# Kernel tuning notes

Measured on AMD Instinct MI355X. Metric: run time of the kernel, lower is better.

## Reference

```python
import jax, jax.numpy as jnp
import numpy as np

K = 16                 # neighbors
CH = (64, 64, 64)      # edge-MLP channels
C_IN = 64              # input feature channels
EPS = 1e-3             # Keras BatchNormalization default epsilon


def setup_inputs() -> dict:
    key = jax.random.key(0)
    ks = jax.random.split(key, 24)
    B, N = 256, 128
    inp = {}
    inp["points"] = jax.random.normal(ks[0], (B, N, 2), jnp.float32)
    inp["features"] = jax.random.normal(ks[1], (B, N, C_IN), jnp.float32)
    ins = [2 * C_IN, CH[0], CH[1]]
    i = 2
    for l, (cin, cout) in enumerate(zip(ins, CH)):
        inp[f"w{l}"] = jax.random.normal(ks[i], (cin, cout), jnp.float32) / np.sqrt(cin).astype(np.float32); i += 1
        inp[f"g{l}"] = jnp.ones((cout,), jnp.float32)
        inp[f"b{l}"] = jnp.zeros((cout,), jnp.float32)
        inp[f"m{l}"] = 0.1 * jax.random.normal(ks[i], (cout,), jnp.float32); i += 1
        inp[f"v{l}"] = jnp.ones((cout,), jnp.float32)
    inp["wsc"] = jax.random.normal(ks[i], (C_IN, CH[-1]), jnp.float32) / np.sqrt(C_IN).astype(np.float32); i += 1
    inp["gsc"] = jnp.ones((CH[-1],), jnp.float32)
    inp["bsc"] = jnp.zeros((CH[-1],), jnp.float32)
    inp["msc"] = 0.1 * jax.random.normal(ks[i], (CH[-1],), jnp.float32)
    inp["vsc"] = jnp.ones((CH[-1],), jnp.float32)
    return inp


def _bn(x, g, b, m, v):
    # inference-mode BatchNorm over last (channel) axis
    return (x - m) * jax.lax.rsqrt(v + EPS) * g + b


def _forward(points, features, params):
    # pairwise squared distances  [B, N, N]
    r = jnp.sum(points * points, axis=-1, keepdims=True)
    d = r - 2.0 * jnp.einsum('bnd,bmd->bnm', points, points) + jnp.swapaxes(r, 1, 2)
    # k+1 nearest (incl. self), drop self  -> [B, N, K]
    _, idx = jax.lax.top_k(-d, K + 1)
    idx = idx[:, :, 1:]
    # gather neighbor features  [B, N, K, C]
    knn = jax.vmap(lambda f, i: f[i])(features, idx)
    center = features[:, :, None, :]
    # edge features: concat(center, neighbor - center)  [B, N, K, 2C]
    x = jnp.concatenate([jnp.broadcast_to(center, knn.shape), knn - center], axis=-1)
    # edge MLP: 1x1 convs == per-edge matmuls
    for (w, g, b, m, v) in params[:-1]:
        x = jax.nn.relu(_bn(jnp.einsum('bnkc,cd->bnkd', x, w), g, b, m, v))
    pooled = jnp.mean(x, axis=2)                      # [B, N, C_out]
    wsc, gsc, bsc, msc, vsc = params[-1]
    sc = _bn(features @ wsc, gsc, bsc, msc, vsc)      # shortcut 1x1 conv + BN
    return jax.nn.relu(sc + pooled)


def reference(points, features,
              w0, g0, b0, m0, v0,
              w1, g1, b1, m1, v1,
              w2, g2, b2, m2, v2,
              wsc, gsc, bsc, msc, vsc):
    params = [(w0, g0, b0, m0, v0), (w1, g1, b1, m1, v1),
              (w2, g2, b2, m2, v2), (wsc, gsc, bsc, msc, vsc)]
    return _forward(points, features, params)
```

## Files before the change

### kernel.cpp

```cpp
#include <hip/hip_runtime.h>
#include <stdint.h>


#define KK 16
#define EPSV 1e-3f
#define SW0 136
#define SW 72

typedef __bf16 bf16x8 __attribute__((ext_vector_type(8)));
typedef float f32x4 __attribute__((ext_vector_type(4)));
union B8 { uint4 u; bf16x8 v; };

__device__ __forceinline__ unsigned int f2ord(float f) {
  unsigned int u = __float_as_uint(f);
  return (u & 0x80000000u) ? ~u : (u | 0x80000000u);
}
__device__ __forceinline__ unsigned int f2b(float f) {
  unsigned int u = __float_as_uint(f);
  return (u + 0x7FFFu + ((u >> 16) & 1u)) >> 16;
}
__device__ __forceinline__ unsigned int pk(float lo, float hi) {
  return f2b(lo) | (f2b(hi) << 16);
}

__global__ __launch_bounds__(256) void knn_kernel(const float* __restrict__ pts,
                                                  int* __restrict__ knn) {
  __shared__ __align__(16) unsigned long long keys[4][128];
  const int wv = threadIdx.x >> 6;
  const int lane = threadIdx.x & 63;
  const int row = blockIdx.x * 4 + wv;
  const int b = row >> 7;
  const int n = row & 127;
  const float* pb = pts + b * 128 * 2;
  const float xn = pb[2 * n], yn = pb[2 * n + 1];
  const float rn = __fadd_rn(__fmul_rn(xn, xn), __fmul_rn(yn, yn));

  unsigned long long key0, key1;
#pragma unroll
  for (int h = 0; h < 2; ++h) {
    const int j = lane + h * 64;
    const float xj = pb[2 * j], yj = pb[2 * j + 1];
    const float rj = __fadd_rn(__fmul_rn(xj, xj), __fmul_rn(yj, yj));
    const float dot = __fadd_rn(__fmul_rn(xn, xj), __fmul_rn(yn, yj));
    const float d = __fadd_rn(__fsub_rn(rn, __fmul_rn(2.0f, dot)), rj);
    unsigned long long k = ((unsigned long long)f2ord(d) << 32) | (unsigned int)j;
    if (h == 0) key0 = k; else key1 = k;
  }
  keys[wv][lane] = key0;
  keys[wv][lane + 64] = key1;
  int c0 = 0, c1 = 0;
#pragma unroll 8
  for (int j = 0; j < 128; j += 2) {
    const ulonglong2 kp = *(const ulonglong2*)&keys[wv][j];
    c0 += (kp.x < key0); c0 += (kp.y < key0);
    c1 += (kp.x < key1); c1 += (kp.y < key1);
  }
  if (c0 >= 1 && c0 <= 16) knn[row * KK + c0 - 1] = lane;
  if (c1 >= 1 && c1 <= 16) knn[row * KK + c1 - 1] = lane + 64;
}

__global__ __launch_bounds__(256, 2) void mlp_kernel(
    const float* __restrict__ feat, const int* __restrict__ knnIdx,
    const float* __restrict__ w0, const float* __restrict__ g0,
    const float* __restrict__ b0, const float* __restrict__ m0,
    const float* __restrict__ v0, const float* __restrict__ w1,
    const float* __restrict__ g1, const float* __restrict__ b1,
    const float* __restrict__ m1, const float* __restrict__ v1,
    const float* __restrict__ w2, const float* __restrict__ g2,
    const float* __restrict__ b2, const float* __restrict__ m2,
    const float* __restrict__ v2, const float* __restrict__ wsc,
    const float* __restrict__ gsc, const float* __restrict__ bsc,
    const float* __restrict__ msc, const float* __restrict__ vsc,
    float* __restrict__ out) {
  __shared__ __align__(16) unsigned short w0T[64 * SW0];
  __shared__ __align__(16) unsigned short w1T[64 * SW];
  __shared__ __align__(16) unsigned short w2T[64 * SW];
  __shared__ __align__(16) unsigned short wscT[64 * SW];
  __shared__ __align__(16) unsigned short X0[4][16 * SW0];
  __shared__ __align__(16) unsigned short CFB[4][16 * SW];

  const int tid = threadIdx.x;
  const int wv = tid >> 6;
  const int lane = tid & 63;
  const int m = lane & 15;
  const int q4 = lane >> 4;

#pragma unroll
  for (int q = 0; q < 8; ++q) {
    const int v = tid + 256 * q;
    const float4 w = ((const float4*)w0)[v];
    const int i = v >> 4, c = (v & 15) << 2;
    w0T[(c + 0) * SW0 + i] = (unsigned short)f2b(w.x);
    w0T[(c + 1) * SW0 + i] = (unsigned short)f2b(w.y);
    w0T[(c + 2) * SW0 + i] = (unsigned short)f2b(w.z);
    w0T[(c + 3) * SW0 + i] = (unsigned short)f2b(w.w);
  }
#pragma unroll
  for (int q = 0; q < 4; ++q) {
    const int v = tid + 256 * q;
    const int i = v >> 4, c = (v & 15) << 2;
    float4 w = ((const float4*)w1)[v];
    w1T[(c + 0) * SW + i] = (unsigned short)f2b(w.x);
    w1T[(c + 1) * SW + i] = (unsigned short)f2b(w.y);
    w1T[(c + 2) * SW + i] = (unsigned short)f2b(w.z);
    w1T[(c + 3) * SW + i] = (unsigned short)f2b(w.w);
    w = ((const float4*)w2)[v];
    w2T[(c + 0) * SW + i] = (unsigned short)f2b(w.x);
    w2T[(c + 1) * SW + i] = (unsigned short)f2b(w.y);
    w2T[(c + 2) * SW + i] = (unsigned short)f2b(w.z);
    w2T[(c + 3) * SW + i] = (unsigned short)f2b(w.w);
    w = ((const float4*)wsc)[v];
    wscT[(c + 0) * SW + i] = (unsigned short)f2b(w.x);
    wscT[(c + 1) * SW + i] = (unsigned short)f2b(w.y);
    wscT[(c + 2) * SW + i] = (unsigned short)f2b(w.z);
    wscT[(c + 3) * SW + i] = (unsigned short)f2b(w.w);
  }

  float s0[4], o0[4], s1[4], o1[4], s2[4], o2[4], ssc[4], osc[4];
#pragma unroll
  for (int nt = 0; nt < 4; ++nt) {
    const int c = nt * 16 + m;
    float s;
    s = g0[c] / sqrtf(v0[c] + EPSV); s0[nt] = s; o0[nt] = b0[c] - m0[c] * s;
    s = g1[c] / sqrtf(v1[c] + EPSV); s1[nt] = s; o1[nt] = b1[c] - m1[c] * s;
    s = g2[c] / sqrtf(v2[c] + EPSV); s2[nt] = s; o2[nt] = b2[c] - m2[c] * s;
    s = gsc[c] / sqrtf(vsc[c] + EPSV); ssc[nt] = s; osc[nt] = bsc[c] - msc[c] * s;
  }

  const int row0 = blockIdx.x * 64 + wv * 16;
  {
    const int r = lane >> 2, p = lane & 3;
    const float4* fr = (const float4*)(feat + (row0 + r) * 64);
    const float4 a = fr[p * 4 + 0], bq = fr[p * 4 + 1];
    const float4 cq = fr[p * 4 + 2], dq = fr[p * 4 + 3];
    uint4 u0, u1;
    u0.x = pk(a.x, a.y); u0.y = pk(a.z, a.w);
    u0.z = pk(bq.x, bq.y); u0.w = pk(bq.z, bq.w);
    u1.x = pk(cq.x, cq.y); u1.y = pk(cq.z, cq.w);
    u1.z = pk(dq.x, dq.y); u1.w = pk(dq.z, dq.w);
    *(uint4*)&CFB[wv][r * SW + p * 16] = u0;
    *(uint4*)&CFB[wv][r * SW + p * 16 + 8] = u1;
  }
  __syncthreads();

  const f32x4 fzero = {0.f, 0.f, 0.f, 0.f};
  f32x4 sacc[4] = {fzero, fzero, fzero, fzero};
#pragma unroll
  for (int t = 0; t < 2; ++t) {
    B8 af; af.u = *(const uint4*)&CFB[wv][m * SW + t * 32 + q4 * 8];
#pragma unroll
    for (int nt = 0; nt < 4; ++nt) {
      B8 bf_; bf_.u = *(const uint4*)&wscT[(nt * 16 + m) * SW + t * 32 + q4 * 8];
      sacc[nt] = __builtin_amdgcn_mfma_f32_16x16x32_bf16(af.v, bf_.v, sacc[nt], 0, 0, 0);
    }
  }
  float scf[4][4];
#pragma unroll
  for (int nt = 0; nt < 4; ++nt)
#pragma unroll
    for (int r = 0; r < 4; ++r)
      scf[nt][r] = fmaf(sacc[nt][r], ssc[nt], osc[nt]);

  const float* featb = feat + (row0 >> 7) * (128 * 64);
  const int kk = lane >> 2, pp = lane & 3;

  for (int qo = 0; qo < 4; ++qo) {
#pragma unroll
    for (int ri = 0; ri < 4; ++ri) {
      const int rr = qo * 4 + ri;
      const int row = row0 + rr;

      {
        const int j = knnIdx[row * KK + kk];
        const float4* np_ = (const float4*)(featb + j * 64);
        const float4* cp_ = (const float4*)(feat + row * 64);
        const float4 n0 = np_[pp * 4 + 0], n1 = np_[pp * 4 + 1];
        const float4 n2 = np_[pp * 4 + 2], n3 = np_[pp * 4 + 3];
        const float4 c0 = cp_[pp * 4 + 0], c1 = cp_[pp * 4 + 1];
        const float4 c2 = cp_[pp * 4 + 2], c3 = cp_[pp * 4 + 3];
        uint4 u;
        u.x = pk(c0.x, c0.y); u.y = pk(c0.z, c0.w);
        u.z = pk(c1.x, c1.y); u.w = pk(c1.z, c1.w);
        *(uint4*)&X0[wv][kk * SW0 + pp * 16] = u;
        u.x = pk(c2.x, c2.y); u.y = pk(c2.z, c2.w);
        u.z = pk(c3.x, c3.y); u.w = pk(c3.z, c3.w);
        *(uint4*)&X0[wv][kk * SW0 + pp * 16 + 8] = u;
        u.x = pk(n0.x - c0.x, n0.y - c0.y); u.y = pk(n0.z - c0.z, n0.w - c0.w);
        u.z = pk(n1.x - c1.x, n1.y - c1.y); u.w = pk(n1.z - c1.z, n1.w - c1.w);
        *(uint4*)&X0[wv][kk * SW0 + 64 + pp * 16] = u;
        u.x = pk(n2.x - c2.x, n2.y - c2.y); u.y = pk(n2.z - c2.z, n2.w - c2.w);
        u.z = pk(n3.x - c3.x, n3.y - c3.y); u.w = pk(n3.z - c3.z, n3.w - c3.w);
        *(uint4*)&X0[wv][kk * SW0 + 64 + pp * 16 + 8] = u;
      }

      f32x4 acc[4] = {fzero, fzero, fzero, fzero};
#pragma unroll
      for (int t = 0; t < 4; ++t) {
        B8 af; af.u = *(const uint4*)&X0[wv][m * SW0 + t * 32 + q4 * 8];
#pragma unroll
        for (int nt = 0; nt < 4; ++nt) {
          B8 bf_; bf_.u = *(const uint4*)&w0T[(nt * 16 + m) * SW0 + t * 32 + q4 * 8];
          acc[nt] = __builtin_amdgcn_mfma_f32_16x16x32_bf16(af.v, bf_.v, acc[nt], 0, 0, 0);
        }
      }
#pragma unroll
      for (int nt = 0; nt < 4; ++nt)
#pragma unroll
        for (int r2 = 0; r2 < 4; ++r2) {
          const float y = fmaxf(fmaf(acc[nt][r2], s0[nt], o0[nt]), 0.f);
          X0[wv][(q4 * 4 + r2) * SW0 + nt * 16 + m] = (unsigned short)f2b(y);
        }

      acc[0] = fzero; acc[1] = fzero; acc[2] = fzero; acc[3] = fzero;
#pragma unroll
      for (int t = 0; t < 2; ++t) {
        B8 af; af.u = *(const uint4*)&X0[wv][m * SW0 + t * 32 + q4 * 8];
#pragma unroll
        for (int nt = 0; nt < 4; ++nt) {
          B8 bf_; bf_.u = *(const uint4*)&w1T[(nt * 16 + m) * SW + t * 32 + q4 * 8];
          acc[nt] = __builtin_amdgcn_mfma_f32_16x16x32_bf16(af.v, bf_.v, acc[nt], 0, 0, 0);
        }
      }
#pragma unroll
      for (int nt = 0; nt < 4; ++nt)
#pragma unroll
        for (int r2 = 0; r2 < 4; ++r2) {
          const float y = fmaxf(fmaf(acc[nt][r2], s1[nt], o1[nt]), 0.f);
          X0[wv][(q4 * 4 + r2) * SW0 + nt * 16 + m] = (unsigned short)f2b(y);
        }

      acc[0] = fzero; acc[1] = fzero; acc[2] = fzero; acc[3] = fzero;
#pragma unroll
      for (int t = 0; t < 2; ++t) {
        B8 af; af.u = *(const uint4*)&X0[wv][m * SW0 + t * 32 + q4 * 8];
#pragma unroll
        for (int nt = 0; nt < 4; ++nt) {
          B8 bf_; bf_.u = *(const uint4*)&w2T[(nt * 16 + m) * SW + t * 32 + q4 * 8];
          acc[nt] = __builtin_amdgcn_mfma_f32_16x16x32_bf16(af.v, bf_.v, acc[nt], 0, 0, 0);
        }
      }

      float pool[4];
#pragma unroll
      for (int nt = 0; nt < 4; ++nt) {
        float p_ = 0.f;
#pragma unroll
        for (int r2 = 0; r2 < 4; ++r2)
          p_ += fmaxf(fmaf(acc[nt][r2], s2[nt], o2[nt]), 0.f);
        p_ += __shfl_xor(p_, 16);
        p_ += __shfl_xor(p_, 32);
        pool[nt] = p_ * 0.0625f;
      }
      if (q4 == qo) {
#pragma unroll
        for (int nt = 0; nt < 4; ++nt)
          out[row * 64 + nt * 16 + m] = fmaxf(scf[nt][ri] + pool[nt], 0.f);
      }
    }
  }
}

extern "C" void kernel_launch(void* const* d_in, const int* in_sizes, int n_in,
                              void* d_out, int out_size, void* d_ws, size_t ws_size,
                              hipStream_t stream) {
  const float* pts = (const float*)d_in[0];
  const float* feat = (const float*)d_in[1];
  const float* w0 = (const float*)d_in[2];
  const float* g0 = (const float*)d_in[3];
  const float* b0 = (const float*)d_in[4];
  const float* m0 = (const float*)d_in[5];
  const float* v0 = (const float*)d_in[6];
  const float* w1 = (const float*)d_in[7];
  const float* g1 = (const float*)d_in[8];
  const float* b1 = (const float*)d_in[9];
  const float* m1 = (const float*)d_in[10];
  const float* v1 = (const float*)d_in[11];
  const float* w2 = (const float*)d_in[12];
  const float* g2 = (const float*)d_in[13];
  const float* b2 = (const float*)d_in[14];
  const float* m2 = (const float*)d_in[15];
  const float* v2 = (const float*)d_in[16];
  const float* wsc = (const float*)d_in[17];
  const float* gsc = (const float*)d_in[18];
  const float* bsc = (const float*)d_in[19];
  const float* msc = (const float*)d_in[20];
  const float* vsc = (const float*)d_in[21];
  float* out = (float*)d_out;

  int* knn = (int*)d_ws;

  knn_kernel<<<dim3(256 * 128 / 4), dim3(256), 0, stream>>>(pts, knn);
  mlp_kernel<<<dim3(512), dim3(256), 0, stream>>>(
      feat, knn, w0, g0, b0, m0, v0, w1, g1, b1, m1, v1, w2, g2, b2, m2, v2,
      wsc, gsc, bsc, msc, vsc, out);
}
```

Measured before the change: 180.9 us.

## Precompute center term of first edge layer once per point and prefetch neighbor rows

The first edge-MLP layer is split algebraically: concat(c, n-c)·W0 = c·(W0top - W0bot) + n·W0bot. The center contribution is computed once per point with MFMA and broadcast by shuffle, so the per-row layer-0 GEMM drops from K=128 to K=64 and the center feature reload per row goes away. kNN indices are loaded up front and the next neighbor row is software-prefetched while the current one is computed. The bf16 conversion now uses the native cast, and the LDS staging buffer shrinks. The neighbor term is rounded to bf16 directly instead of the difference, which slightly changes numerics, and more registers stay live.

```diff
diff --git a/kernel.cpp b/kernel.cpp
--- a/kernel.cpp
+++ b/kernel.cpp
@@ -15,12 +15,12 @@
   unsigned int u = __float_as_uint(f);
   return (u & 0x80000000u) ? ~u : (u | 0x80000000u);
 }
-__device__ __forceinline__ unsigned int f2b(float f) {
-  unsigned int u = __float_as_uint(f);
-  return (u + 0x7FFFu + ((u >> 16) & 1u)) >> 16;
+__device__ __forceinline__ unsigned short f2bs(float f) {
+  __bf16 b = (__bf16)f;
+  return __builtin_bit_cast(unsigned short, b);
 }
 __device__ __forceinline__ unsigned int pk(float lo, float hi) {
-  return f2b(lo) | (f2b(hi) << 16);
+  return (unsigned int)f2bs(lo) | ((unsigned int)f2bs(hi) << 16);
 }
 
 __global__ __launch_bounds__(256) void knn_kernel(const float* __restrict__ pts,
@@ -31,17 +31,17 @@
   const int row = blockIdx.x * 4 + wv;
   const int b = row >> 7;
   const int n = row & 127;
-  const float* pb = pts + b * 128 * 2;
-  const float xn = pb[2 * n], yn = pb[2 * n + 1];
-  const float rn = __fadd_rn(__fmul_rn(xn, xn), __fmul_rn(yn, yn));
+  const float2* pb = (const float2*)(pts + b * 128 * 2);
+  const float2 pn = pb[n];
+  const float rn = __fadd_rn(__fmul_rn(pn.x, pn.x), __fmul_rn(pn.y, pn.y));
 
   unsigned long long key0, key1;
 #pragma unroll
   for (int h = 0; h < 2; ++h) {
     const int j = lane + h * 64;
-    const float xj = pb[2 * j], yj = pb[2 * j + 1];
-    const float rj = __fadd_rn(__fmul_rn(xj, xj), __fmul_rn(yj, yj));
-    const float dot = __fadd_rn(__fmul_rn(xn, xj), __fmul_rn(yn, yj));
+    const float2 pj = pb[j];
+    const float rj = __fadd_rn(__fmul_rn(pj.x, pj.x), __fmul_rn(pj.y, pj.y));
+    const float dot = __fadd_rn(__fmul_rn(pn.x, pj.x), __fmul_rn(pn.y, pj.y));
     const float d = __fadd_rn(__fsub_rn(rn, __fmul_rn(2.0f, dot)), rj);
     unsigned long long k = ((unsigned long long)f2ord(d) << 32) | (unsigned int)j;
     if (h == 0) key0 = k; else key1 = k;
@@ -76,8 +76,7 @@
   __shared__ __align__(16) unsigned short w1T[64 * SW];
   __shared__ __align__(16) unsigned short w2T[64 * SW];
   __shared__ __align__(16) unsigned short wscT[64 * SW];
-  __shared__ __align__(16) unsigned short X0[4][16 * SW0];
-  __shared__ __align__(16) unsigned short CFB[4][16 * SW];
+  __shared__ __align__(16) unsigned short X0[4][16 * SW];
 
   const int tid = threadIdx.x;
   const int wv = tid >> 6;
@@ -90,30 +89,30 @@
     const int v = tid + 256 * q;
     const float4 w = ((const float4*)w0)[v];
     const int i = v >> 4, c = (v & 15) << 2;
-    w0T[(c + 0) * SW0 + i] = (unsigned short)f2b(w.x);
-    w0T[(c + 1) * SW0 + i] = (unsigned short)f2b(w.y);
-    w0T[(c + 2) * SW0 + i] = (unsigned short)f2b(w.z);
-    w0T[(c + 3) * SW0 + i] = (unsigned short)f2b(w.w);
+    w0T[(c + 0) * SW0 + i] = f2bs(w.x);
+    w0T[(c + 1) * SW0 + i] = f2bs(w.y);
+    w0T[(c + 2) * SW0 + i] = f2bs(w.z);
+    w0T[(c + 3) * SW0 + i] = f2bs(w.w);
   }
 #pragma unroll
   for (int q = 0; q < 4; ++q) {
     const int v = tid + 256 * q;
     const int i = v >> 4, c = (v & 15) << 2;
     float4 w = ((const float4*)w1)[v];
-    w1T[(c + 0) * SW + i] = (unsigned short)f2b(w.x);
-    w1T[(c + 1) * SW + i] = (unsigned short)f2b(w.y);
-    w1T[(c + 2) * SW + i] = (unsigned short)f2b(w.z);
-    w1T[(c + 3) * SW + i] = (unsigned short)f2b(w.w);
+    w1T[(c + 0) * SW + i] = f2bs(w.x);
+    w1T[(c + 1) * SW + i] = f2bs(w.y);
+    w1T[(c + 2) * SW + i] = f2bs(w.z);
+    w1T[(c + 3) * SW + i] = f2bs(w.w);
     w = ((const float4*)w2)[v];
-    w2T[(c + 0) * SW + i] = (unsigned short)f2b(w.x);
-    w2T[(c + 1) * SW + i] = (unsigned short)f2b(w.y);
-    w2T[(c + 2) * SW + i] = (unsigned short)f2b(w.z);
-    w2T[(c + 3) * SW + i] = (unsigned short)f2b(w.w);
+    w2T[(c + 0) * SW + i] = f2bs(w.x);
+    w2T[(c + 1) * SW + i] = f2bs(w.y);
+    w2T[(c + 2) * SW + i] = f2bs(w.z);
+    w2T[(c + 3) * SW + i] = f2bs(w.w);
     w = ((const float4*)wsc)[v];
-    wscT[(c + 0) * SW + i] = (unsigned short)f2b(w.x);
-    wscT[(c + 1) * SW + i] = (unsigned short)f2b(w.y);
-    wscT[(c + 2) * SW + i] = (unsigned short)f2b(w.z);
-    wscT[(c + 3) * SW + i] = (unsigned short)f2b(w.w);
+    wscT[(c + 0) * SW + i] = f2bs(w.x);
+    wscT[(c + 1) * SW + i] = f2bs(w.y);
+    wscT[(c + 2) * SW + i] = f2bs(w.z);
+    wscT[(c + 3) * SW + i] = f2bs(w.w);
   }
 
   float s0[4], o0[4], s1[4], o1[4], s2[4], o2[4], ssc[4], osc[4];
@@ -128,6 +127,12 @@
   }
 
   const int row0 = blockIdx.x * 64 + wv * 16;
+  const int kk = lane >> 2, pp = lane & 3;
+
+  int jdx[16];
+#pragma unroll
+  for (int rr = 0; rr < 16; ++rr) jdx[rr] = knnIdx[(row0 + rr) * KK + kk];
+
   {
     const int r = lane >> 2, p = lane & 3;
     const float4* fr = (const float4*)(feat + (row0 + r) * 64);
@@ -138,124 +143,135 @@
     u0.z = pk(bq.x, bq.y); u0.w = pk(bq.z, bq.w);
     u1.x = pk(cq.x, cq.y); u1.y = pk(cq.z, cq.w);
     u1.z = pk(dq.x, dq.y); u1.w = pk(dq.z, dq.w);
-    *(uint4*)&CFB[wv][r * SW + p * 16] = u0;
-    *(uint4*)&CFB[wv][r * SW + p * 16 + 8] = u1;
-  }
+    *(uint4*)&X0[wv][r * SW + p * 16] = u0;
+    *(uint4*)&X0[wv][r * SW + p * 16 + 8] = u1;
+  }
+
+  const float* featb = feat + (row0 >> 7) * (128 * 64);
+  float4 n0, n1, n2, n3;
+  {
+    const float4* np_ = (const float4*)(featb + jdx[0] * 64);
+    n0 = np_[pp * 4 + 0]; n1 = np_[pp * 4 + 1];
+    n2 = np_[pp * 4 + 2]; n3 = np_[pp * 4 + 3];
+  }
+
   __syncthreads();
 
   const f32x4 fzero = {0.f, 0.f, 0.f, 0.f};
   f32x4 sacc[4] = {fzero, fzero, fzero, fzero};
+  f32x4 ctp[4] = {fzero, fzero, fzero, fzero};
+  f32x4 cbt[4] = {fzero, fzero, fzero, fzero};
 #pragma unroll
   for (int t = 0; t < 2; ++t) {
-    B8 af; af.u = *(const uint4*)&CFB[wv][m * SW + t * 32 + q4 * 8];
+    B8 af; af.u = *(const uint4*)&X0[wv][m * SW + t * 32 + q4 * 8];
 #pragma unroll
     for (int nt = 0; nt < 4; ++nt) {
-      B8 bf_; bf_.u = *(const uint4*)&wscT[(nt * 16 + m) * SW + t * 32 + q4 * 8];
-      sacc[nt] = __builtin_amdgcn_mfma_f32_16x16x32_bf16(af.v, bf_.v, sacc[nt], 0, 0, 0);
-    }
-  }
-  float scf[4][4];
+      B8 bs, bt, bb;
+      bs.u = *(const uint4*)&wscT[(nt * 16 + m) * SW + t * 32 + q4 * 8];
+      bt.u = *(const uint4*)&w0T[(nt * 16 + m) * SW0 + t * 32 + q4 * 8];
+      bb.u = *(const uint4*)&w0T[(nt * 16 + m) * SW0 + 64 + t * 32 + q4 * 8];
+      sacc[nt] = __builtin_amdgcn_mfma_f32_16x16x32_bf16(af.v, bs.v, sacc[nt], 0, 0, 0);
+      ctp[nt]  = __builtin_amdgcn_mfma_f32_16x16x32_bf16(af.v, bt.v, ctp[nt], 0, 0, 0);
+      cbt[nt]  = __builtin_amdgcn_mfma_f32_16x16x32_bf16(af.v, bb.v, cbt[nt], 0, 0, 0);
+    }
+  }
+  float scf[4][4], ct[4][4];
 #pragma unroll
   for (int nt = 0; nt < 4; ++nt)
 #pragma unroll
-    for (int r = 0; r < 4; ++r)
+    for (int r = 0; r < 4; ++r) {
       scf[nt][r] = fmaf(sacc[nt][r], ssc[nt], osc[nt]);
-
-  const float* featb = feat + (row0 >> 7) * (128 * 64);
-  const int kk = lane >> 2, pp = lane & 3;
-
-  for (int qo = 0; qo < 4; ++qo) {
-#pragma unroll
-    for (int ri = 0; ri < 4; ++ri) {
-      const int rr = qo * 4 + ri;
-      const int row = row0 + rr;
-
-      {
-        const int j = knnIdx[row * KK + kk];
-        const float4* np_ = (const float4*)(featb + j * 64);
-        const float4* cp_ = (const float4*)(feat + row * 64);
-        const float4 n0 = np_[pp * 4 + 0], n1 = np_[pp * 4 + 1];
-        const float4 n2 = np_[pp * 4 + 2], n3 = np_[pp * 4 + 3];
-        const float4 c0 = cp_[pp * 4 + 0], c1 = cp_[pp * 4 + 1];
-        const float4 c2 = cp_[pp * 4 + 2], c3 = cp_[pp * 4 + 3];
-        uint4 u;
-        u.x = pk(c0.x, c0.y); u.y = pk(c0.z, c0.w);
-        u.z = pk(c1.x, c1.y); u.w = pk(c1.z, c1.w);
-        *(uint4*)&X0[wv][kk * SW0 + pp * 16] = u;
-        u.x = pk(c2.x, c2.y); u.y = pk(c2.z, c2.w);
-        u.z = pk(c3.x, c3.y); u.w = pk(c3.z, c3.w);
-        *(uint4*)&X0[wv][kk * SW0 + pp * 16 + 8] = u;
-        u.x = pk(n0.x - c0.x, n0.y - c0.y); u.y = pk(n0.z - c0.z, n0.w - c0.w);
-        u.z = pk(n1.x - c1.x, n1.y - c1.y); u.w = pk(n1.z - c1.z, n1.w - c1.w);
-        *(uint4*)&X0[wv][kk * SW0 + 64 + pp * 16] = u;
-        u.x = pk(n2.x - c2.x, n2.y - c2.y); u.y = pk(n2.z - c2.z, n2.w - c2.w);
-        u.z = pk(n3.x - c3.x, n3.y - c3.y); u.w = pk(n3.z - c3.z, n3.w - c3.w);
-        *(uint4*)&X0[wv][kk * SW0 + 64 + pp * 16 + 8] = u;
-      }
-
-      f32x4 acc[4] = {fzero, fzero, fzero, fzero};
-#pragma unroll
-      for (int t = 0; t < 4; ++t) {
-        B8 af; af.u = *(const uint4*)&X0[wv][m * SW0 + t * 32 + q4 * 8];
-#pragma unroll
-        for (int nt = 0; nt < 4; ++nt) {
-          B8 bf_; bf_.u = *(const uint4*)&w0T[(nt * 16 + m) * SW0 + t * 32 + q4 * 8];
-          acc[nt] = __builtin_amdgcn_mfma_f32_16x16x32_bf16(af.v, bf_.v, acc[nt], 0, 0, 0);
-        }
-      }
+      ct[nt][r] = ctp[nt][r] - cbt[nt][r];
+    }
+
+#pragma unroll
+  for (int rr = 0; rr < 16; ++rr) {
+    const int qo = rr >> 2, ri = rr & 3;
+    const int row = row0 + rr;
+
+    {
+      uint4 u;
+      u.x = pk(n0.x, n0.y); u.y = pk(n0.z, n0.w);
+      u.z = pk(n1.x, n1.y); u.w = pk(n1.z, n1.w);
+      *(uint4*)&X0[wv][kk * SW + pp * 16] = u;
+      u.x = pk(n2.x, n2.y); u.y = pk(n2.z, n2.w);
+      u.z = pk(n3.x, n3.y); u.w = pk(n3.z, n3.w);
+      *(uint4*)&X0[wv][kk * SW + pp * 16 + 8] = u;
+    }
+    if (rr < 15) {
+      const float4* np_ = (const float4*)(featb + jdx[rr + 1] * 64);
+      n0 = np_[pp * 4 + 0]; n1 = np_[pp * 4 + 1];
+      n2 = np_[pp * 4 + 2]; n3 = np_[pp * 4 + 3];
+    }
+
+    f32x4 acc[4];
+#pragma unroll
+    for (int nt = 0; nt < 4; ++nt) {
+      const float ci = __shfl(ct[nt][ri], qo * 16 + m);
+      f32x4 a; a[0] = ci; a[1] = ci; a[2] = ci; a[3] = ci;
+      acc[nt] = a;
+    }
+#pragma unroll
+    for (int t = 0; t < 2; ++t) {
+      B8 af; af.u = *(const uint4*)&X0[wv][m * SW + t * 32 + q4 * 8];
+#pragma unroll
+      for (int nt = 0; nt < 4; ++nt) {
+        B8 bf_; bf_.u = *(const uint4*)&w0T[(nt * 16 + m) * SW0 + 64 + t * 32 + q4 * 8];
+        acc[nt] = __builtin_amdgcn_mfma_f32_16x16x32_bf16(af.v, bf_.v, acc[nt], 0, 0, 0);
+      }
+    }
+#pragma unroll
+    for (int nt = 0; nt < 4; ++nt)
+#pragma unroll
+      for (int r2 = 0; r2 < 4; ++r2) {
+        const float y = fmaxf(fmaf(acc[nt][r2], s0[nt], o0[nt]), 0.f);
+        X0[wv][(q4 * 4 + r2) * SW + nt * 16 + m] = f2bs(y);
+      }
+
+    acc[0] = fzero; acc[1] = fzero; acc[2] = fzero; acc[3] = fzero;
+#pragma unroll
+    for (int t = 0; t < 2; ++t) {
+      B8 af; af.u = *(const uint4*)&X0[wv][m * SW + t * 32 + q4 * 8];
+#pragma unroll
+      for (int nt = 0; nt < 4; ++nt) {
+        B8 bf_; bf_.u = *(const uint4*)&w1T[(nt * 16 + m) * SW + t * 32 + q4 * 8];
+        acc[nt] = __builtin_amdgcn_mfma_f32_16x16x32_bf16(af.v, bf_.v, acc[nt], 0, 0, 0);
+      }
+    }
+#pragma unroll
+    for (int nt = 0; nt < 4; ++nt)
+#pragma unroll
+      for (int r2 = 0; r2 < 4; ++r2) {
+        const float y = fmaxf(fmaf(acc[nt][r2], s1[nt], o1[nt]), 0.f);
+        X0[wv][(q4 * 4 + r2) * SW + nt * 16 + m] = f2bs(y);
+      }
+
+    acc[0] = fzero; acc[1] = fzero; acc[2] = fzero; acc[3] = fzero;
+#pragma unroll
+    for (int t = 0; t < 2; ++t) {
+      B8 af; af.u = *(const uint4*)&X0[wv][m * SW + t * 32 + q4 * 8];
+#pragma unroll
+      for (int nt = 0; nt < 4; ++nt) {
+        B8 bf_; bf_.u = *(const uint4*)&w2T[(nt * 16 + m) * SW + t * 32 + q4 * 8];
+        acc[nt] = __builtin_amdgcn_mfma_f32_16x16x32_bf16(af.v, bf_.v, acc[nt], 0, 0, 0);
+      }
+    }
+
+    float pool[4];
+#pragma unroll
+    for (int nt = 0; nt < 4; ++nt) {
+      float p_ = 0.f;
+#pragma unroll
+      for (int r2 = 0; r2 < 4; ++r2)
+        p_ += fmaxf(fmaf(acc[nt][r2], s2[nt], o2[nt]), 0.f);
+      p_ += __shfl_xor(p_, 16);
+      p_ += __shfl_xor(p_, 32);
+      pool[nt] = p_ * 0.0625f;
+    }
+    if (q4 == qo) {
 #pragma unroll
       for (int nt = 0; nt < 4; ++nt)
-#pragma unroll
-        for (int r2 = 0; r2 < 4; ++r2) {
-          const float y = fmaxf(fmaf(acc[nt][r2], s0[nt], o0[nt]), 0.f);
-          X0[wv][(q4 * 4 + r2) * SW0 + nt * 16 + m] = (unsigned short)f2b(y);
-        }
-
-      acc[0] = fzero; acc[1] = fzero; acc[2] = fzero; acc[3] = fzero;
-#pragma unroll
-      for (int t = 0; t < 2; ++t) {
-        B8 af; af.u = *(const uint4*)&X0[wv][m * SW0 + t * 32 + q4 * 8];
-#pragma unroll
-        for (int nt = 0; nt < 4; ++nt) {
-          B8 bf_; bf_.u = *(const uint4*)&w1T[(nt * 16 + m) * SW + t * 32 + q4 * 8];
-          acc[nt] = __builtin_amdgcn_mfma_f32_16x16x32_bf16(af.v, bf_.v, acc[nt], 0, 0, 0);
-        }
-      }
-#pragma unroll
-      for (int nt = 0; nt < 4; ++nt)
-#pragma unroll
-        for (int r2 = 0; r2 < 4; ++r2) {
-          const float y = fmaxf(fmaf(acc[nt][r2], s1[nt], o1[nt]), 0.f);
-          X0[wv][(q4 * 4 + r2) * SW0 + nt * 16 + m] = (unsigned short)f2b(y);
-        }
-
-      acc[0] = fzero; acc[1] = fzero; acc[2] = fzero; acc[3] = fzero;
-#pragma unroll
-      for (int t = 0; t < 2; ++t) {
-        B8 af; af.u = *(const uint4*)&X0[wv][m * SW0 + t * 32 + q4 * 8];
-#pragma unroll
-        for (int nt = 0; nt < 4; ++nt) {
-          B8 bf_; bf_.u = *(const uint4*)&w2T[(nt * 16 + m) * SW + t * 32 + q4 * 8];
-          acc[nt] = __builtin_amdgcn_mfma_f32_16x16x32_bf16(af.v, bf_.v, acc[nt], 0, 0, 0);
-        }
-      }
-
-      float pool[4];
-#pragma unroll
-      for (int nt = 0; nt < 4; ++nt) {
-        float p_ = 0.f;
-#pragma unroll
-        for (int r2 = 0; r2 < 4; ++r2)
-          p_ += fmaxf(fmaf(acc[nt][r2], s2[nt], o2[nt]), 0.f);
-        p_ += __shfl_xor(p_, 16);
-        p_ += __shfl_xor(p_, 32);
-        pool[nt] = p_ * 0.0625f;
-      }
-      if (q4 == qo) {
-#pragma unroll
-        for (int nt = 0; nt < 4; ++nt)
-          out[row * 64 + nt * 16 + m] = fmaxf(scf[nt][ri] + pool[nt], 0.f);
-      }
+        out[row * 64 + nt * 16 + m] = fmaxf(scf[nt][ri] + pool[nt], 0.f);
     }
   }
 }
```

Result: faster. 171.8 us (-5.0%).
